# Kernel tuning notes

Hardware: AMD Instinct MI355X
Metric: run time of the kernel (lower is better)

## Reference

```python
import jax, jax.numpy as jnp
import numpy as np

N_ATOMS = 50000
N_PAIRS = 800000
N_EMB = 128
N_DIST = 100
N_HID = 128


def _glorot(key, shape):
    scale = jnp.sqrt(2.0 / (shape[0] + shape[1])).astype(jnp.float32)
    return jax.random.normal(key, shape, dtype=jnp.float32) * scale


def setup_inputs() -> dict:
    key = jax.random.key(0)
    ks = jax.random.split(key, 10)
    atom_features = jax.random.normal(ks[0], (N_ATOMS, N_EMB), dtype=jnp.float32)
    distance = jax.random.uniform(ks[1], (N_PAIRS, N_DIST), dtype=jnp.float32)
    atom_membership = jax.random.randint(ks[2], (N_ATOMS,), 0, 64, dtype=jnp.int32)
    distance_membership_i = jnp.sort(
        jax.random.randint(ks[3], (N_PAIRS,), 0, N_ATOMS, dtype=jnp.int32))
    distance_membership_j = jax.random.randint(ks[4], (N_PAIRS,), 0, N_ATOMS, dtype=jnp.int32)
    W_cf = _glorot(ks[5], (N_EMB, N_HID))
    W_df = _glorot(ks[6], (N_DIST, N_HID))
    W_fc = _glorot(ks[7], (N_HID, N_EMB))
    # original inits biases to zero; use small random so the b_df*afh branch is non-trivial
    b_cf = jax.random.normal(ks[8], (N_HID,), dtype=jnp.float32) * 0.1
    b_df = jax.random.normal(ks[9], (N_HID,), dtype=jnp.float32) * 0.1
    return {
        "atom_features": atom_features,
        "distance": distance,
        "atom_membership": atom_membership,
        "distance_membership_i": distance_membership_i,
        "distance_membership_j": distance_membership_j,
        "W_cf": W_cf, "W_df": W_df, "W_fc": W_fc,
        "b_cf": b_cf, "b_df": b_df,
    }


def reference(atom_features, distance, atom_membership,
              distance_membership_i, distance_membership_j,
              W_cf, W_df, W_fc, b_cf, b_df):
    n_atoms = atom_features.shape[0]
    # [n_pairs, n_hidden]
    distance_hidden = distance @ W_df + b_df
    # [n_atoms, n_hidden]
    atom_features_hidden = atom_features @ W_cf + b_cf
    # gather source-atom hidden feats per pair, fuse with distance feats
    msgs = distance_hidden * atom_features_hidden[distance_membership_j]
    msgs = jnp.tanh(msgs @ W_fc)                      # [n_pairs, n_emb]
    # self-interaction correction term
    output_ii = jnp.tanh((b_df * atom_features_hidden) @ W_fc)  # [n_atoms, n_emb]
    agg = jax.ops.segment_sum(msgs, distance_membership_i, num_segments=n_atoms)
    return agg - output_ii + atom_features
```

## Files before the change

kernel.cpp:

```cpp
#include <hip/hip_runtime.h>
#include <hip/hip_bf16.h>

#define N_ATOMS 50000
#define N_PAIRS 800000
#define N_EMB   128
#define N_DIST  100
#define N_HID   128
#define TP      128

typedef __attribute__((ext_vector_type(8))) short bf16x8;
typedef __attribute__((ext_vector_type(4))) float f32x4;

__device__ __forceinline__ short f2b(float x) {
  union { float f; unsigned u; } v; v.f = x;
  unsigned r = (v.u + 0x7FFF + ((v.u >> 16) & 1)) >> 16;
  return (short)r;
}
__device__ __forceinline__ float b2f(short b) {
  union { unsigned u; float f; } v; v.u = ((unsigned)(unsigned short)b) << 16;
  return v.f;
}
__device__ __forceinline__ float fast_tanh(float x) {
  const float z = __builtin_amdgcn_exp2f(x * 2.8853900817779268f);
  return 1.f - 2.f * __builtin_amdgcn_rcpf(z + 1.f);
}

__device__ __forceinline__ int frag_idx(int k, int n) {
  return ((((k >> 5) * 8 + (n >> 4)) * 64) + (((k >> 3) & 3) * 16) + (n & 15)) * 8 + (k & 7);
}

__device__ __forceinline__ void g2lds16(const void* g, void* l) {
  __builtin_amdgcn_global_load_lds(
      (const __attribute__((address_space(1))) unsigned*)g,
      (__attribute__((address_space(3))) unsigned*)l, 16, 0, 0);
}
__device__ __forceinline__ void stage_weights(const short* __restrict__ src,
                                              short* WS, int tid) {
  #pragma unroll
  for (int r = 0; r < 4; ++r) {
    const int off = (r * 512 + tid) * 8;
    g2lds16(src + off, WS + off);
  }
}

__global__ __launch_bounds__(256) void prep_kernel(
    const float* __restrict__ Wcf, const float* __restrict__ Wdf,
    const float* __restrict__ Wfc, short* __restrict__ Wcf_f,
    short* __restrict__ Wdf_f, short* __restrict__ Wfc_f) {
  const int e = blockIdx.x * 256 + threadIdx.x;
  const int k = e >> 7, n = e & 127;
  const int fi = frag_idx(k, n);
  Wcf_f[fi] = f2b(Wcf[k * N_HID + n]);
  Wfc_f[fi] = f2b(Wfc[k * N_EMB + n]);
  Wdf_f[fi] = (k < N_DIST) ? f2b(Wdf[k * N_HID + n]) : (short)0;
}

__global__ __launch_bounds__(512) void afh_kernel(
    const float* __restrict__ af, const short* __restrict__ Wcf_f,
    const float* __restrict__ bcf, float* __restrict__ afh) {
  __shared__ short WS[128 * 128];
  const int tid = threadIdx.x;
  const int lane = tid & 63, w = tid >> 6;
  const int lane15 = lane & 15, quad = lane >> 4;
  const int a0 = blockIdx.x * 128;

  stage_weights(Wcf_f, WS, tid);

  f32x4 acc[8];
  #pragma unroll
  for (int nt = 0; nt < 8; ++nt) {
    const float b = bcf[nt * 16 + lane15];
    acc[nt] = (f32x4){b, b, b, b};
  }
  const int arow = min(a0 + w * 16 + lane15, N_ATOMS - 1);
  const float* __restrict__ p = af + (long)arow * N_EMB;
  __syncthreads();

  for (int ks = 0; ks < 4; ++ks) {
    const int k0 = ks * 32 + quad * 8;
    const float4 x = *(const float4*)(p + k0);
    const float4 y = *(const float4*)(p + k0 + 4);
    bf16x8 a;
    a[0] = f2b(x.x); a[1] = f2b(x.y); a[2] = f2b(x.z); a[3] = f2b(x.w);
    a[4] = f2b(y.x); a[5] = f2b(y.y); a[6] = f2b(y.z); a[7] = f2b(y.w);
    #pragma unroll
    for (int nt = 0; nt < 8; ++nt) {
      const bf16x8 b = *(const bf16x8*)&WS[((ks * 8 + nt) * 64 + lane) * 8];
      acc[nt] = __builtin_amdgcn_mfma_f32_16x16x32_bf16(a, b, acc[nt], 0, 0, 0);
    }
  }
  #pragma unroll
  for (int reg = 0; reg < 4; ++reg) {
    const int row = a0 + w * 16 + quad * 4 + reg;
    if (row < N_ATOMS) {
      #pragma unroll
      for (int nt = 0; nt < 8; ++nt)
        afh[(long)row * N_HID + nt * 16 + lane15] = acc[nt][reg];
    }
  }
}

__global__ __launch_bounds__(512, 4) void pair_kernel(
    const float* __restrict__ dist, const int* __restrict__ mi,
    const int* __restrict__ mj, const short* __restrict__ Wdf_f,
    const short* __restrict__ Wfc_f, const float* __restrict__ bdf,
    const float* __restrict__ afh, float* __restrict__ agg) {
  __shared__ short WS[128 * 128];
  __shared__ short HS[TP * 128];

  const int tid = threadIdx.x;
  const int lane = tid & 63;
  const int w = tid >> 6;
  const int lane15 = lane & 15;
  const int quad = lane >> 4;
  const long pbase = (long)blockIdx.x * TP;
  const int R = w * 16;

  stage_weights(Wdf_f, WS, tid);

  f32x4 acc[8];
  #pragma unroll
  for (int nt = 0; nt < 8; ++nt) {
    const float b = bdf[nt * 16 + lane15];
    acc[nt] = (f32x4){b, b, b, b};
  }
  const float* __restrict__ drow = dist + (pbase + R + lane15) * (long)N_DIST;
  __syncthreads();

  for (int ks = 0; ks < 4; ++ks) {
    bf16x8 a;
    const int k0 = ks * 32 + quad * 8;
    if (ks < 3) {
      const float4 x = *(const float4*)(drow + k0);
      const float4 y = *(const float4*)(drow + k0 + 4);
      a[0] = f2b(x.x); a[1] = f2b(x.y); a[2] = f2b(x.z); a[3] = f2b(x.w);
      a[4] = f2b(y.x); a[5] = f2b(y.y); a[6] = f2b(y.z); a[7] = f2b(y.w);
    } else {
      #pragma unroll
      for (int j = 0; j < 8; ++j)
        a[j] = (k0 + j < N_DIST) ? f2b(drow[k0 + j]) : (short)0;
    }
    #pragma unroll
    for (int nt = 0; nt < 8; ++nt) {
      const bf16x8 b = *(const bf16x8*)&WS[((ks * 8 + nt) * 64 + lane) * 8];
      acc[nt] = __builtin_amdgcn_mfma_f32_16x16x32_bf16(a, b, acc[nt], 0, 0, 0);
    }
  }
  __syncthreads();

  stage_weights(Wfc_f, WS, tid);

  #pragma unroll
  for (int reg = 0; reg < 4; ++reg) {
    const int r = R + quad * 4 + reg;
    const long j = mj[pbase + r];
    const float* __restrict__ arow = afh + j * N_HID;
    #pragma unroll
    for (int nt = 0; nt < 8; ++nt) {
      const int col = nt * 16 + lane15;
      const float h = acc[nt][reg] * arow[col];
      const int ch = (col >> 3) ^ (r & 15);
      HS[(r << 7) + (ch << 3) + (col & 7)] = f2b(h);
    }
  }
  __syncthreads();

  f32x4 acc2[8];
  #pragma unroll
  for (int nt = 0; nt < 8; ++nt) acc2[nt] = (f32x4){0.f, 0.f, 0.f, 0.f};
  const int m = R + lane15;
  for (int ks = 0; ks < 4; ++ks) {
    const int ch = (ks * 4 + quad) ^ lane15;
    const bf16x8 a = *(const bf16x8*)&HS[(m << 7) + (ch << 3)];
    #pragma unroll
    for (int nt = 0; nt < 8; ++nt) {
      const bf16x8 b = *(const bf16x8*)&WS[((ks * 8 + nt) * 64 + lane) * 8];
      acc2[nt] = __builtin_amdgcn_mfma_f32_16x16x32_bf16(a, b, acc2[nt], 0, 0, 0);
    }
  }

  #pragma unroll
  for (int reg = 0; reg < 4; ++reg) {
    const int r = R + quad * 4 + reg;
    #pragma unroll
    for (int nt = 0; nt < 8; ++nt) {
      const int col = nt * 16 + lane15;
      const float tv = fast_tanh(acc2[nt][reg]);
      const int ch = (col >> 3) ^ (r & 15);
      HS[(r << 7) + (ch << 3) + (col & 7)] = f2b(tv);
    }
  }
  __syncthreads();

  {
    const int col = tid & 127;
    const int seg = tid >> 7;
    const int r0 = seg * 32;
    float s = 0.f;
    int cur = mi[pbase + r0];
    for (int rr = 0; rr < 32; ++rr) {
      const int r = r0 + rr;
      const int idx = mi[pbase + r];
      if (idx != cur) {
        atomicAdd(&agg[(size_t)cur * N_EMB + col], s);
        s = 0.f; cur = idx;
      }
      const int ch = (col >> 3) ^ (r & 15);
      s += b2f(HS[(r << 7) + (ch << 3) + (col & 7)]);
    }
    atomicAdd(&agg[(size_t)cur * N_EMB + col], s);
  }
}

__global__ __launch_bounds__(512) void out_kernel(
    const float* __restrict__ af, const float* __restrict__ afh,
    const short* __restrict__ Wfc_f, const float* __restrict__ bdf,
    const float* __restrict__ agg, float* __restrict__ out) {
  __shared__ short WS[128 * 128];
  const int tid = threadIdx.x;
  const int lane = tid & 63, w = tid >> 6;
  const int lane15 = lane & 15, quad = lane >> 4;
  const int a0 = blockIdx.x * 128;

  stage_weights(Wfc_f, WS, tid);

  f32x4 acc[8];
  #pragma unroll
  for (int nt = 0; nt < 8; ++nt) acc[nt] = (f32x4){0.f, 0.f, 0.f, 0.f};
  const int arow = min(a0 + w * 16 + lane15, N_ATOMS - 1);
  const float* __restrict__ p = afh + (long)arow * N_HID;
  __syncthreads();

  for (int ks = 0; ks < 4; ++ks) {
    const int k0 = ks * 32 + quad * 8;
    const float4 x = *(const float4*)(p + k0);
    const float4 y = *(const float4*)(p + k0 + 4);
    const float4 bx = *(const float4*)(bdf + k0);
    const float4 by = *(const float4*)(bdf + k0 + 4);
    bf16x8 a;
    a[0] = f2b(x.x * bx.x); a[1] = f2b(x.y * bx.y);
    a[2] = f2b(x.z * bx.z); a[3] = f2b(x.w * bx.w);
    a[4] = f2b(y.x * by.x); a[5] = f2b(y.y * by.y);
    a[6] = f2b(y.z * by.z); a[7] = f2b(y.w * by.w);
    #pragma unroll
    for (int nt = 0; nt < 8; ++nt) {
      const bf16x8 b = *(const bf16x8*)&WS[((ks * 8 + nt) * 64 + lane) * 8];
      acc[nt] = __builtin_amdgcn_mfma_f32_16x16x32_bf16(a, b, acc[nt], 0, 0, 0);
    }
  }
  #pragma unroll
  for (int reg = 0; reg < 4; ++reg) {
    const int row = a0 + w * 16 + quad * 4 + reg;
    if (row < N_ATOMS) {
      #pragma unroll
      for (int nt = 0; nt < 8; ++nt) {
        const size_t idx = (size_t)row * N_EMB + nt * 16 + lane15;
        out[idx] = agg[idx] - fast_tanh(acc[nt][reg]) + af[idx];
      }
    }
  }
}

extern "C" void kernel_launch(void* const* d_in, const int* in_sizes, int n_in,
                              void* d_out, int out_size, void* d_ws, size_t ws_size,
                              hipStream_t stream) {
  const float* af   = (const float*)d_in[0];
  const float* dist = (const float*)d_in[1];
  const int*   mi   = (const int*)d_in[3];
  const int*   mj   = (const int*)d_in[4];
  const float* Wcf  = (const float*)d_in[5];
  const float* Wdf  = (const float*)d_in[6];
  const float* Wfc  = (const float*)d_in[7];
  const float* bcf  = (const float*)d_in[8];
  const float* bdf  = (const float*)d_in[9];
  float* out = (float*)d_out;

  float* afh = (float*)d_ws;
  float* agg = afh + (size_t)N_ATOMS * N_HID;
  short* Wcf_f = (short*)(agg + (size_t)N_ATOMS * N_EMB);
  short* Wdf_f = Wcf_f + 128 * 128;
  short* Wfc_f = Wdf_f + 128 * 128;

  hipMemsetAsync(agg, 0, (size_t)N_ATOMS * N_EMB * sizeof(float), stream);
  prep_kernel<<<64, 256, 0, stream>>>(Wcf, Wdf, Wfc, Wcf_f, Wdf_f, Wfc_f);
  afh_kernel<<<(N_ATOMS + 127) / 128, 512, 0, stream>>>(af, Wcf_f, bcf, afh);
  pair_kernel<<<N_PAIRS / TP, 512, 0, stream>>>(dist, mi, mj, Wdf_f, Wfc_f, bdf, afh, agg);
  out_kernel<<<(N_ATOMS + 127) / 128, 512, 0, stream>>>(af, afh, Wfc_f, bdf, agg, out);
}
```

Before: 619.4 us.

## Prefetch gathers and distance rows early, use per-wave segmented reduction

Issues the afh gather loads and all distance row loads before the weight-staging barrier so their latency overlaps with staging and the first GEMM. The final segment-sum is restructured so each wave reduces its own 16 rows, two columns per lane, which lets a wave barrier replace the block-wide __syncthreads. This raises register pressure (32 gathered floats plus 8 float4 per thread) under launch_bounds(512,4). Per-wave reduction over 16 rows instead of 32 can roughly double the number of atomics issued.

```diff
diff --git a/kernel.cpp b/kernel.cpp
--- a/kernel.cpp
+++ b/kernel.cpp
@@ -118,28 +118,46 @@
 
   stage_weights(Wdf_f, WS, tid);
 
+  float g[4][8];
+  #pragma unroll
+  for (int reg = 0; reg < 4; ++reg) {
+    const int r = R + quad * 4 + reg;
+    const long j = mj[pbase + r];
+    const float* __restrict__ arow = afh + j * N_HID + lane15;
+    #pragma unroll
+    for (int nt = 0; nt < 8; ++nt)
+      g[reg][nt] = arow[nt * 16];
+  }
+
+  const float* __restrict__ drow = dist + (pbase + R + lane15) * (long)N_DIST;
+  float4 dx[4], dy[4];
+  #pragma unroll
+  for (int ks = 0; ks < 3; ++ks) {
+    const int k0 = ks * 32 + quad * 8;
+    dx[ks] = *(const float4*)(drow + k0);
+    dy[ks] = *(const float4*)(drow + k0 + 4);
+  }
+  {
+    const float4 z = {0.f, 0.f, 0.f, 0.f};
+    dx[3] = (quad == 0) ? *(const float4*)(drow + 96) : z;
+    dy[3] = z;
+  }
+
   f32x4 acc[8];
   #pragma unroll
   for (int nt = 0; nt < 8; ++nt) {
     const float b = bdf[nt * 16 + lane15];
     acc[nt] = (f32x4){b, b, b, b};
   }
-  const float* __restrict__ drow = dist + (pbase + R + lane15) * (long)N_DIST;
-  __syncthreads();
-
+  __syncthreads();
+
+  #pragma unroll
   for (int ks = 0; ks < 4; ++ks) {
     bf16x8 a;
-    const int k0 = ks * 32 + quad * 8;
-    if (ks < 3) {
-      const float4 x = *(const float4*)(drow + k0);
-      const float4 y = *(const float4*)(drow + k0 + 4);
-      a[0] = f2b(x.x); a[1] = f2b(x.y); a[2] = f2b(x.z); a[3] = f2b(x.w);
-      a[4] = f2b(y.x); a[5] = f2b(y.y); a[6] = f2b(y.z); a[7] = f2b(y.w);
-    } else {
-      #pragma unroll
-      for (int j = 0; j < 8; ++j)
-        a[j] = (k0 + j < N_DIST) ? f2b(drow[k0 + j]) : (short)0;
-    }
+    a[0] = f2b(dx[ks].x); a[1] = f2b(dx[ks].y);
+    a[2] = f2b(dx[ks].z); a[3] = f2b(dx[ks].w);
+    a[4] = f2b(dy[ks].x); a[5] = f2b(dy[ks].y);
+    a[6] = f2b(dy[ks].z); a[7] = f2b(dy[ks].w);
     #pragma unroll
     for (int nt = 0; nt < 8; ++nt) {
       const bf16x8 b = *(const bf16x8*)&WS[((ks * 8 + nt) * 64 + lane) * 8];
@@ -153,12 +171,10 @@
   #pragma unroll
   for (int reg = 0; reg < 4; ++reg) {
     const int r = R + quad * 4 + reg;
-    const long j = mj[pbase + r];
-    const float* __restrict__ arow = afh + j * N_HID;
     #pragma unroll
     for (int nt = 0; nt < 8; ++nt) {
       const int col = nt * 16 + lane15;
-      const float h = acc[nt][reg] * arow[col];
+      const float h = acc[nt][reg] * g[reg][nt];
       const int ch = (col >> 3) ^ (r & 15);
       HS[(r << 7) + (ch << 3) + (col & 7)] = f2b(h);
     }
@@ -169,6 +185,7 @@
   #pragma unroll
   for (int nt = 0; nt < 8; ++nt) acc2[nt] = (f32x4){0.f, 0.f, 0.f, 0.f};
   const int m = R + lane15;
+  #pragma unroll
   for (int ks = 0; ks < 4; ++ks) {
     const int ch = (ks * 4 + quad) ^ lane15;
     const bf16x8 a = *(const bf16x8*)&HS[(m << 7) + (ch << 3)];
@@ -190,25 +207,29 @@
       HS[(r << 7) + (ch << 3) + (col & 7)] = f2b(tv);
     }
   }
-  __syncthreads();
+  __builtin_amdgcn_wave_barrier();
 
   {
-    const int col = tid & 127;
-    const int seg = tid >> 7;
-    const int r0 = seg * 32;
-    float s = 0.f;
-    int cur = mi[pbase + r0];
-    for (int rr = 0; rr < 32; ++rr) {
-      const int r = r0 + rr;
-      const int idx = mi[pbase + r];
+    const int c0 = lane * 2;
+    const long p0 = pbase + R;
+    float s0 = 0.f, s1 = 0.f;
+    int cur = mi[p0];
+    for (int rr = 0; rr < 16; ++rr) {
+      const int r = R + rr;
+      const int idx = mi[p0 + rr];
       if (idx != cur) {
-        atomicAdd(&agg[(size_t)cur * N_EMB + col], s);
-        s = 0.f; cur = idx;
+        atomicAdd(&agg[(size_t)cur * N_EMB + c0], s0);
+        atomicAdd(&agg[(size_t)cur * N_EMB + c0 + 1], s1);
+        s0 = s1 = 0.f; cur = idx;
       }
-      const int ch = (col >> 3) ^ (r & 15);
-      s += b2f(HS[(r << 7) + (ch << 3) + (col & 7)]);
-    }
-    atomicAdd(&agg[(size_t)cur * N_EMB + col], s);
+      const int ch = (c0 >> 3) ^ (r & 15);
+      const unsigned v =
+          *(const unsigned*)&HS[(r << 7) + (ch << 3) + (c0 & 7)];
+      s0 += b2f((short)(v & 0xFFFF));
+      s1 += b2f((short)(v >> 16));
+    }
+    atomicAdd(&agg[(size_t)cur * N_EMB + c0], s0);
+    atomicAdd(&agg[(size_t)cur * N_EMB + c0 + 1], s1);
   }
 }
 
```

Result: faster. 601.5 us (-2.9%).
